# Kernel optimization log

Hardware: AMD Instinct MI355X
Metric: run time of the kernel (lower is better)

## Reference

```python
import jax, jax.numpy as jnp
import numpy as np

B, H, W = 16, 56, 56
CE, CB = 128, 256
NH, WS = 8, 7
HD = CB // NH
N = WS * WS
HID = 4 * CB
EPS = 1e-5


def _rel_pos_index(ws):
    coords = np.stack(np.meshgrid(np.arange(ws), np.arange(ws), indexing='ij')).reshape(2, -1)
    rel = (coords[:, :, None] - coords[:, None, :]).transpose(1, 2, 0).astype(np.int64)
    rel[..., 0] += ws - 1
    rel[..., 1] += ws - 1
    rel[..., 0] *= 2 * ws - 1
    return rel.sum(-1)  # (ws*ws, ws*ws)

RPI = jnp.asarray(_rel_pos_index(WS))


def _ln(x, w, b, axes):
    m = x.mean(axes, keepdims=True)
    v = x.var(axes, keepdims=True)
    return (x - m) * jax.lax.rsqrt(v + EPS) * w + b


def _window_partition(x):  # (B,H,W,C) -> (B*nW, N, C)
    Bx, Hx, Wx, C = x.shape
    x = x.reshape(Bx, Hx // WS, WS, Wx // WS, WS, C)
    return x.transpose(0, 1, 3, 2, 4, 5).reshape(-1, N, C)


def _window_reverse(xw, C):  # (B*nW, N, C) -> (B,H,W,C)
    x = xw.reshape(B, H // WS, W // WS, WS, WS, C)
    return x.transpose(0, 1, 3, 2, 4, 5).reshape(B, H, W, C)


def setup_inputs() -> dict:
    key = jax.random.key(0)
    ks = jax.random.split(key, 12)
    s = 0.02
    return {
        'x_edge': jax.random.normal(ks[0], (B, CE, H, W), jnp.float32),
        'x_body': jax.random.normal(ks[1], (B, H * W, CB), jnp.float32),
        'norm_edge_w': jnp.ones((CE, H, W), jnp.float32),
        'norm_edge_b': jnp.zeros((CE, H, W), jnp.float32),
        'conv_w': jax.random.normal(ks[2], (CB, CE), jnp.float32) * s,
        'norm1_w': jnp.ones((CB,), jnp.float32),
        'norm1_b': jnp.zeros((CB,), jnp.float32),
        'rpb_table': jax.random.normal(ks[3], ((2 * WS - 1) ** 2, NH), jnp.float32) * s,
        'q_w': jax.random.normal(ks[4], (CB, CB), jnp.float32) * s,
        'kv_w': jax.random.normal(ks[5], (2 * CB, CB), jnp.float32) * s,
        'proj_w': jax.random.normal(ks[6], (CB, CB), jnp.float32) * s,
        'proj_b': jnp.zeros((CB,), jnp.float32),
        'norm2_w': jnp.ones((CB,), jnp.float32),
        'norm2_b': jnp.zeros((CB,), jnp.float32),
        'fc1_w': jax.random.normal(ks[7], (HID, CB), jnp.float32) * s,
        'fc1_b': jnp.zeros((HID,), jnp.float32),
        'fc2_w': jax.random.normal(ks[8], (CB, HID), jnp.float32) * s,
        'fc2_b': jnp.zeros((CB,), jnp.float32),
    }


def reference(x_edge, x_body, norm_edge_w, norm_edge_b, conv_w, norm1_w, norm1_b,
              rpb_table, q_w, kv_w, proj_w, proj_b, norm2_w, norm2_b,
              fc1_w, fc1_b, fc2_w, fc2_b):
    x_body_cache = x_body
    scale = HD ** -0.5

    # LayerNorm over (C,H,W) of x_edge, then 1x1 conv (channel mixing), to NHWC
    xe = _ln(x_edge, norm_edge_w, norm_edge_b, axes=(1, 2, 3))  # (B,CE,H,W)
    xe = jnp.einsum('oc,bchw->bhwo', conv_w, xe)                # (B,H,W,CB)

    xb = _ln(x_body, norm1_w, norm1_b, axes=(-1,)).reshape(B, H, W, CB)

    xe_w = _window_partition(xe)  # (Bn,N,CB)
    xb_w = _window_partition(xb)

    q = (xe_w @ q_w.T).reshape(-1, N, NH, HD).transpose(0, 2, 1, 3) * scale  # (Bn,NH,N,HD)
    kv = (xb_w @ kv_w.T).reshape(-1, N, 2, NH, HD).transpose(2, 0, 3, 1, 4)
    k, v = kv[0], kv[1]  # (Bn,NH,N,HD)

    attn = jnp.einsum('bhnd,bhmd->bhnm', q, k)
    bias = rpb_table[RPI.reshape(-1)].reshape(N, N, NH).transpose(2, 0, 1)  # (NH,N,N)
    attn = jax.nn.softmax(attn + bias[None], axis=-1)

    out = jnp.einsum('bhnm,bhmd->bhnd', attn, v).transpose(0, 2, 1, 3).reshape(-1, N, CB)
    out = out @ proj_w.T + proj_b

    x_attn = _window_reverse(out, CB).reshape(B, H * W, CB)
    x = x_body_cache + x_attn

    h = _ln(x, norm2_w, norm2_b, axes=(-1,))
    h = jax.nn.gelu(h @ fc1_w.T + fc1_b, approximate=False) @ fc2_w.T + fc2_b
    x = x + h

    return x.reshape(B, H, W, CB).transpose(0, 3, 1, 2)  # (B,CB,H,W)
```

## Files before the change

kernel.cpp:

```cpp
#include <hip/hip_runtime.h>
#include <hip/hip_bf16.h>
#include <math.h>

#define B_    16
#define CE_   128
#define CB_   256
#define H_    56
#define W_    56
#define NH_   8
#define WS_   7
#define HD_   32
#define NWIN_ 49
#define HW_   3136
#define M_    50176
#define HID_  1024

typedef short bf16x8 __attribute__((ext_vector_type(8)));
typedef float f32x4  __attribute__((ext_vector_type(4)));

__device__ __forceinline__ float waveRedSum(float v) {
#pragma unroll
  for (int off = 32; off; off >>= 1) v += __shfl_xor(v, off, 64);
  return v;
}

__device__ __forceinline__ void load_lds16(const void* g, void* l) {
  __builtin_amdgcn_global_load_lds((__attribute__((address_space(1))) void*)g,
                                   (__attribute__((address_space(3))) void*)l,
                                   16, 0, 0);
}

__global__ void k_stats1(const float* __restrict__ xe, float* __restrict__ part) {
  int blk = blockIdx.x;
  int b = blk >> 6, s = blk & 63;
  const float4* p = (const float4*)(xe + (size_t)b * 401408 + s * 6272);
  float sm = 0.f, s2 = 0.f;
  for (int i = threadIdx.x; i < 1568; i += 256) {
    float4 v = p[i];
    sm += v.x + v.y + v.z + v.w;
    s2 += v.x * v.x + v.y * v.y + v.z * v.z + v.w * v.w;
  }
  sm = waveRedSum(sm); s2 = waveRedSum(s2);
  __shared__ float aux[8];
  int wave = threadIdx.x >> 6, lane = threadIdx.x & 63;
  if (lane == 0) { aux[wave] = sm; aux[4 + wave] = s2; }
  __syncthreads();
  if (threadIdx.x == 0) {
    part[blk * 2]     = aux[0] + aux[1] + aux[2] + aux[3];
    part[blk * 2 + 1] = aux[4] + aux[5] + aux[6] + aux[7];
  }
}

__global__ void k_stats2(const float* __restrict__ part, float* __restrict__ stats) {
  int b = blockIdx.x, lane = threadIdx.x;
  float sm = part[(b * 64 + lane) * 2];
  float s2 = part[(b * 64 + lane) * 2 + 1];
  sm = waveRedSum(sm); s2 = waveRedSum(s2);
  if (lane == 0) {
    float mean = sm / 401408.0f;
    float var  = s2 / 401408.0f - mean * mean;
    stats[b * 2] = mean;
    stats[b * 2 + 1] = rsqrtf(var + 1e-5f);
  }
}

__global__ void k_cast6(const float* __restrict__ s0, const float* __restrict__ s1,
                        const float* __restrict__ s2, const float* __restrict__ s3,
                        const float* __restrict__ s4, const float* __restrict__ s5,
                        __hip_bfloat16* __restrict__ d) {
  size_t i4 = ((size_t)blockIdx.x * 256 + threadIdx.x) * 4;
  if (i4 >= 819200) return;
  const float* src; size_t off;
  if      (i4 < 32768)  { src = s0; off = 0; }
  else if (i4 < 98304)  { src = s1; off = 32768; }
  else if (i4 < 229376) { src = s2; off = 98304; }
  else if (i4 < 294912) { src = s3; off = 229376; }
  else if (i4 < 557056) { src = s4; off = 294912; }
  else                  { src = s5; off = 557056; }
  float4 v = *(const float4*)(src + (i4 - off));
  union { __hip_bfloat16 h[4]; uint2 u; } pk;
  pk.h[0] = __float2bfloat16(v.x);
  pk.h[1] = __float2bfloat16(v.y);
  pk.h[2] = __float2bfloat16(v.z);
  pk.h[3] = __float2bfloat16(v.w);
  *(uint2*)(d + i4) = pk.u;
}

__global__ void k_wqc(const float* __restrict__ qw, const float* __restrict__ cw,
                      __hip_bfloat16* __restrict__ wqc) {
  int o2 = blockIdx.x, c = threadIdx.x;
  float acc = 0.f;
#pragma unroll 4
  for (int o = 0; o < 256; ++o)
    acc += qw[o2 * 256 + o] * cw[o * 128 + c];
  wqc[o2 * 128 + c] = __float2bfloat16(acc * 0.17677669529663687f);
}

__global__ void k_bias_pre(const float* __restrict__ rpb, float* __restrict__ bp) {
  int blk = blockIdx.x;
  int h = blk >> 4, tile = blk & 15;
  int ti = tile >> 2, tj = tile & 3;
  int lane = threadIdx.x;
  int quad = lane >> 4, lm = lane & 15;
  float4 v;
  float* vp = (float*)&v;
#pragma unroll
  for (int r = 0; r < 4; ++r) {
    int i = ti * 16 + quad * 4 + r;
    int j = tj * 16 + lm;
    float b = -1e30f;
    if (i < 49 && j < 49) {
      int rel = (i / 7 - j / 7 + 6) * 13 + (i % 7 - j % 7 + 6);
      b = rpb[rel * 8 + h];
    }
    vp[r] = b;
  }
  *(float4*)&bp[(size_t)(blk * 64 + lane) * 4] = v;
}

__global__ void k_prep_edge(const float* __restrict__ xe,
                            const float* __restrict__ we,
                            const float* __restrict__ be,
                            const float* __restrict__ stats,
                            __hip_bfloat16* __restrict__ Ae) {
  int wb = blockIdx.x;
  int b = wb >> 6, rem = wb & 63;
  int h0 = (rem >> 3) * 7, w0 = (rem & 7) * 7;
  float mean = stats[b * 2], rstd = stats[b * 2 + 1];
  __shared__ __hip_bfloat16 t[49 * 130];
  for (int idx = threadIdx.x; idx < 128 * 49; idx += 256) {
    int c = idx / 49, p = idx % 49;
    int h = h0 + p / 7, w = w0 + p % 7;
    int off = (c * 56 + h) * 56 + w;
    float v = xe[(size_t)b * 401408 + off];
    t[p * 130 + c] = __float2bfloat16((v - mean) * rstd * we[off] + be[off]);
  }
  __syncthreads();
  __hip_bfloat16* dst = Ae + (size_t)wb * 49 * 128;
  for (int idx = threadIdx.x; idx < 49 * 128; idx += 256) {
    int p = idx >> 7, c = idx & 127;
    dst[idx] = t[p * 130 + c];
  }
}

template <bool PERM>
__global__ void k_ln_rows(const float* __restrict__ x,
                          const float* __restrict__ w,
                          const float* __restrict__ bia,
                          __hip_bfloat16* __restrict__ out) {
  int row = blockIdx.x * 4 + (threadIdx.x >> 6);
  int lane = threadIdx.x & 63;
  float4 xv = *(const float4*)(x + (size_t)row * 256 + lane * 4);
  float s  = xv.x + xv.y + xv.z + xv.w;
  float s2 = xv.x * xv.x + xv.y * xv.y + xv.z * xv.z + xv.w * xv.w;
  s = waveRedSum(s); s2 = waveRedSum(s2);
  float mean = s * (1.0f / 256.0f);
  float var  = s2 * (1.0f / 256.0f) - mean * mean;
  float rstd = rsqrtf(var + 1e-5f);
  int orow = row;
  if (PERM) {
    int b = row / 3136, hw = row % 3136;
    int h = hw / 56, ww = hw % 56;
    orow = (b * 64 + (h / 7) * 8 + (ww / 7)) * 49 + (h % 7) * 7 + (ww % 7);
  }
  float4 wv = *(const float4*)(w + lane * 4);
  float4 bv = *(const float4*)(bia + lane * 4);
  union { __hip_bfloat16 h[4]; uint2 u; } pk;
  pk.h[0] = __float2bfloat16((xv.x - mean) * rstd * wv.x + bv.x);
  pk.h[1] = __float2bfloat16((xv.y - mean) * rstd * wv.y + bv.y);
  pk.h[2] = __float2bfloat16((xv.z - mean) * rstd * wv.z + bv.z);
  pk.h[3] = __float2bfloat16((xv.w - mean) * rstd * wv.w + bv.w);
  *(uint2*)(out + (size_t)orow * 256 + lane * 4) = pk.u;
}

template <int EPI, int NX>
__launch_bounds__(256)
__global__ void gemm_bt(const __hip_bfloat16* __restrict__ A,
                        const __hip_bfloat16* __restrict__ Bw,
                        int M, int N, int K,
                        __hip_bfloat16* __restrict__ outb,
                        float* __restrict__ outf,
                        const float* __restrict__ bias,
                        const float* __restrict__ resid) {
  __shared__ __align__(16) char smem[32768];
  __hip_bfloat16* As0 = (__hip_bfloat16*)smem;
  __hip_bfloat16* Bs0 = (__hip_bfloat16*)(smem + 16384);
  const int tid  = threadIdx.x;
  const int lane = tid & 63;
  const int wave = tid >> 6;
  const int quad = lane >> 4;
  const int lm   = lane & 15;
  const int wm   = (wave & 1) << 6;
  const int wn   = (wave >> 1) << 6;
  const int lin  = blockIdx.x;
  const int slot = lin >> 3;
  const int band = (lin & 7) * 49 + slot / NX;
  const int n0   = (slot % NX) * 128;
  const int m0   = band * 128;

  const int rh = (wave & 1) * 64;
  const int qw = wave >> 1;
  const __hip_bfloat16* Arow = A  + (size_t)(m0 + rh + lane) * K;
  const __hip_bfloat16* Brow = Bw + (size_t)(n0 + rh + lane) * K;

  f32x4 acc[4][4];
#pragma unroll
  for (int i = 0; i < 4; ++i)
#pragma unroll
    for (int j = 0; j < 4; ++j)
#pragma unroll
      for (int r = 0; r < 4; ++r) acc[i][j][r] = 0.f;

  auto STAGE = [&](int buf, int k0) {
#pragma unroll
    for (int p = 0; p < 2; ++p) {
      int q = qw + 2 * p;
      load_lds16(Arow + k0 + q * 8, As0 + buf * 4096 + (q * 128 + rh) * 8);
      load_lds16(Brow + k0 + q * 8, Bs0 + buf * 4096 + (q * 128 + rh) * 8);
    }
  };

  const int nt = K >> 5;
  STAGE(0, 0);
  asm volatile("s_waitcnt vmcnt(0)" ::: "memory");
  __builtin_amdgcn_s_barrier();
  __builtin_amdgcn_sched_barrier(0);

  int cur = 0;
  for (int t = 0; t < nt; ++t) {
    if (t + 1 < nt) STAGE(cur ^ 1, (t + 1) << 5);
    bf16x8 af[4], bfr[4];
#pragma unroll
    for (int i = 0; i < 4; ++i)
      af[i] = *(const bf16x8*)(As0 + cur * 4096 + (quad * 128 + wm + i * 16 + lm) * 8);
#pragma unroll
    for (int j = 0; j < 4; ++j)
      bfr[j] = *(const bf16x8*)(Bs0 + cur * 4096 + (quad * 128 + wn + j * 16 + lm) * 8);
#pragma unroll
    for (int i = 0; i < 4; ++i)
#pragma unroll
      for (int j = 0; j < 4; ++j)
        acc[i][j] = __builtin_amdgcn_mfma_f32_16x16x32_bf16(af[i], bfr[j], acc[i][j], 0, 0, 0);
    if (t + 1 < nt) {
      asm volatile("s_waitcnt vmcnt(0)" ::: "memory");
      __builtin_amdgcn_s_barrier();
      __builtin_amdgcn_sched_barrier(0);
    }
    cur ^= 1;
  }

  float* R = (float*)smem;
  const int g    = tid >> 5;
  const int lx   = tid & 31;
  const int half = wave & 1;
  const int gncol = n0 + lx * 4;
  float4 b4;
  if constexpr (EPI != 0) b4 = *(const float4*)&bias[gncol];

#pragma unroll
  for (int i = 0; i < 4; ++i) {
    __syncthreads();
#pragma unroll
    for (int r = 0; r < 4; ++r) {
      const int rl = half * 16 + quad * 4 + r;
#pragma unroll
      for (int j = 0; j < 4; ++j)
        R[rl * 132 + wn + j * 16 + lm] = acc[i][j][r];
    }
    __syncthreads();
#pragma unroll
    for (int p = 0; p < 4; ++p) {
      const int rl = p * 8 + g;
      f32x4 v4 = *(const f32x4*)&R[rl * 132 + lx * 4];
      const int gm = m0 + (rl >> 4) * 64 + i * 16 + (rl & 15);
      if constexpr (EPI == 0) {
        union { __hip_bfloat16 h[4]; uint2 u; } pk;
#pragma unroll
        for (int q2 = 0; q2 < 4; ++q2) pk.h[q2] = __float2bfloat16(v4[q2]);
        *(uint2*)&outb[(size_t)gm * N + gncol] = pk.u;
      } else if constexpr (EPI == 3) {
        union { __hip_bfloat16 h[4]; uint2 u; } pk;
        const float* bp4 = (const float*)&b4;
#pragma unroll
        for (int q2 = 0; q2 < 4; ++q2) {
          float x = v4[q2] + bp4[q2];
          float t = x * fmaf(x * x, -0.10294324f, -2.30220837f);
          float e = __builtin_amdgcn_exp2f(t);
          pk.h[q2] = __float2bfloat16(x * __builtin_amdgcn_rcpf(1.0f + e));
        }
        *(uint2*)&outb[(size_t)gm * N + gncol] = pk.u;
      } else {
        size_t rowbase;
        if constexpr (EPI == 2) {
          int wb = gm / 49, nn = gm % 49;
          int b = wb >> 6, rem = wb & 63;
          int h = (rem >> 3) * 7 + nn / 7, w = (rem & 7) * 7 + nn % 7;
          rowbase = (size_t)(b * 3136 + h * 56 + w) * 256;
        } else {
          rowbase = (size_t)gm * N;
        }
        float4 r4 = *(const float4*)&resid[rowbase + gncol];
        float4 o4;
        o4.x = v4[0] + b4.x + r4.x;
        o4.y = v4[1] + b4.y + r4.y;
        o4.z = v4[2] + b4.z + r4.z;
        o4.w = v4[3] + b4.w + r4.w;
        *(float4*)&outf[rowbase + gncol] = o4;
      }
    }
  }
}

__launch_bounds__(64)
__global__ void k_attn_mfma(const __hip_bfloat16* __restrict__ qb,
                            const __hip_bfloat16* __restrict__ kvb,
                            const float* __restrict__ bp,
                            __hip_bfloat16* __restrict__ ob) {
  int wb = blockIdx.x >> 3;
  int h  = blockIdx.x & 7;
  __shared__ __align__(16) __hip_bfloat16 lds[7424];
  __hip_bfloat16* Qs = lds;
  __hip_bfloat16* Ks = lds + 2560;
  __hip_bfloat16* Vt = lds + 5120;
  __hip_bfloat16* Ps = lds;
  const int lane = threadIdx.x;
  const int quad = lane >> 4, lm = lane & 15;

  const __hip_bfloat16 zb = __float2bfloat16(0.f);
  for (int i = lane; i < 600; i += 64) { Qs[1960 + i] = zb; Ks[1960 + i] = zb; }
  {
    uint4 z; z.x = z.y = z.z = z.w = 0u;
    for (int i = lane; i < 288; i += 64) ((uint4*)Vt)[i] = z;
  }
  {
    int t = lane >> 2, p = lane & 3;
#pragma unroll
    for (int pass = 0; pass < 4; ++pass, t += 16) {
      if (t < 49) {
        size_t rq = (size_t)(wb * 49 + t);
        uint4 qv = *(const uint4*)(qb + rq * 256 + h * 32 + p * 8);
        *(uint4*)&Qs[t * 40 + p * 8] = qv;
        uint4 kv = *(const uint4*)(kvb + rq * 512 + h * 32 + p * 8);
        *(uint4*)&Ks[t * 40 + p * 8] = kv;
        union { uint4 u; __hip_bfloat16 e[8]; } vv;
        vv.u = *(const uint4*)(kvb + rq * 512 + 256 + h * 32 + p * 8);
#pragma unroll
        for (int i = 0; i < 8; ++i) Vt[(p * 8 + i) * 72 + t] = vv.e[i];
      }
    }
  }
  __builtin_amdgcn_s_waitcnt(0);

  bf16x8 qf[4], kf[4];
#pragma unroll
  for (int i = 0; i < 4; ++i) qf[i] = *(const bf16x8*)&Qs[(i * 16 + lm) * 40 + quad * 8];
#pragma unroll
  for (int j = 0; j < 4; ++j) kf[j] = *(const bf16x8*)&Ks[(j * 16 + lm) * 40 + quad * 8];
  f32x4 s[4][4];
#pragma unroll
  for (int i = 0; i < 4; ++i)
#pragma unroll
    for (int j = 0; j < 4; ++j) {
      f32x4 z4; z4[0] = z4[1] = z4[2] = z4[3] = 0.f;
      s[i][j] = __builtin_amdgcn_mfma_f32_16x16x32_bf16(qf[i], kf[j], z4, 0, 0, 0);
    }
#pragma unroll
  for (int ti = 0; ti < 4; ++ti)
#pragma unroll
    for (int tj = 0; tj < 4; ++tj) {
      f32x4 b = *(const f32x4*)&bp[(size_t)(((h * 4 + ti) * 4 + tj) * 64 + lane) * 4];
      s[ti][tj] += b;
    }
  float mrow[4][4], srow[4][4];
#pragma unroll
  for (int ti = 0; ti < 4; ++ti)
#pragma unroll
    for (int r = 0; r < 4; ++r)
      mrow[ti][r] = fmaxf(fmaxf(s[ti][0][r], s[ti][1][r]), fmaxf(s[ti][2][r], s[ti][3][r]));
#pragma unroll
  for (int mask = 1; mask <= 8; mask <<= 1)
#pragma unroll
    for (int ti = 0; ti < 4; ++ti)
#pragma unroll
      for (int r = 0; r < 4; ++r)
        mrow[ti][r] = fmaxf(mrow[ti][r], __shfl_xor(mrow[ti][r], mask, 64));
#pragma unroll
  for (int ti = 0; ti < 4; ++ti)
#pragma unroll
    for (int tj = 0; tj < 4; ++tj)
#pragma unroll
      for (int r = 0; r < 4; ++r)
        s[ti][tj][r] = __expf(s[ti][tj][r] - mrow[ti][r]);
#pragma unroll
  for (int ti = 0; ti < 4; ++ti)
#pragma unroll
    for (int r = 0; r < 4; ++r)
      srow[ti][r] = s[ti][0][r] + s[ti][1][r] + s[ti][2][r] + s[ti][3][r];
#pragma unroll
  for (int mask = 1; mask <= 8; mask <<= 1)
#pragma unroll
    for (int ti = 0; ti < 4; ++ti)
#pragma unroll
      for (int r = 0; r < 4; ++r)
        srow[ti][r] += __shfl_xor(srow[ti][r], mask, 64);
  float inv[4][4];
#pragma unroll
  for (int ti = 0; ti < 4; ++ti)
#pragma unroll
    for (int r = 0; r < 4; ++r)
      inv[ti][r] = 1.0f / srow[ti][r];

#pragma unroll
  for (int ti = 0; ti < 4; ++ti)
#pragma unroll
    for (int tj = 0; tj < 4; ++tj)
#pragma unroll
      for (int r = 0; r < 4; ++r)
        Ps[(ti * 16 + quad * 4 + r) * 72 + tj * 16 + lm] = __float2bfloat16(s[ti][tj][r]);
  __builtin_amdgcn_s_waitcnt(0);

  f32x4 o[4][2];
#pragma unroll
  for (int mt = 0; mt < 4; ++mt)
#pragma unroll
    for (int nt = 0; nt < 2; ++nt)
#pragma unroll
      for (int r = 0; r < 4; ++r) o[mt][nt][r] = 0.f;
#pragma unroll
  for (int kq = 0; kq < 2; ++kq) {
    bf16x8 pa[4], vb[2];
#pragma unroll
    for (int mt = 0; mt < 4; ++mt)
      pa[mt] = *(const bf16x8*)&Ps[(mt * 16 + lm) * 72 + kq * 32 + quad * 8];
#pragma unroll
    for (int nt = 0; nt < 2; ++nt)
      vb[nt] = *(const bf16x8*)&Vt[(nt * 16 + lm) * 72 + kq * 32 + quad * 8];
#pragma unroll
    for (int mt = 0; mt < 4; ++mt)
#pragma unroll
      for (int nt = 0; nt < 2; ++nt)
        o[mt][nt] = __builtin_amdgcn_mfma_f32_16x16x32_bf16(pa[mt], vb[nt], o[mt][nt], 0, 0, 0);
  }
#pragma unroll
  for (int mt = 0; mt < 4; ++mt)
#pragma unroll
    for (int r = 0; r < 4; ++r) {
      int row = mt * 16 + quad * 4 + r;
      if (row < 49) {
#pragma unroll
        for (int nt = 0; nt < 2; ++nt)
          ob[(size_t)(wb * 49 + row) * 256 + h * 32 + nt * 16 + lm] =
              __float2bfloat16(o[mt][nt][r] * inv[mt][r]);
      }
    }
}

__global__ void k_transpose(const float* __restrict__ y, float* __restrict__ out) {
  __shared__ float t[32][33];
  int bb = blockIdx.z;
  int hw0 = blockIdx.x * 32;
  int o0 = blockIdx.y * 32;
  int tx = threadIdx.x, ty = threadIdx.y;
#pragma unroll
  for (int r = 0; r < 4; ++r)
    t[ty + r * 8][tx] = y[(size_t)(bb * 3136 + hw0 + ty + r * 8) * 256 + o0 + tx];
  __syncthreads();
#pragma unroll
  for (int r = 0; r < 4; ++r)
    out[(size_t)(bb * 256 + o0 + ty + r * 8) * 3136 + hw0 + tx] = t[tx][ty + r * 8];
}

extern "C" void kernel_launch(void* const* d_in, const int* in_sizes, int n_in,
                              void* d_out, int out_size, void* d_ws, size_t ws_size,
                              hipStream_t stream) {
  const float* x_edge = (const float*)d_in[0];
  const float* x_body = (const float*)d_in[1];
  const float* ne_w   = (const float*)d_in[2];
  const float* ne_b   = (const float*)d_in[3];
  const float* conv_w = (const float*)d_in[4];
  const float* n1_w   = (const float*)d_in[5];
  const float* n1_b   = (const float*)d_in[6];
  const float* rpb    = (const float*)d_in[7];
  const float* q_w    = (const float*)d_in[8];
  const float* kv_w   = (const float*)d_in[9];
  const float* proj_w = (const float*)d_in[10];
  const float* proj_b = (const float*)d_in[11];
  const float* n2_w   = (const float*)d_in[12];
  const float* n2_b   = (const float*)d_in[13];
  const float* fc1_w  = (const float*)d_in[14];
  const float* fc1_b  = (const float*)d_in[15];
  const float* fc2_w  = (const float*)d_in[16];
  const float* fc2_b  = (const float*)d_in[17];
  float* out = (float*)d_out;
  (void)in_sizes; (void)n_in; (void)out_size; (void)ws_size;

  const size_t SZ_Ae    = (size_t)M_ * 128 * 2;
  const size_t SZ_bf256 = (size_t)M_ * 256 * 2;
  const size_t SZ_bf512 = (size_t)M_ * 512 * 2;
  const size_t SZ_h1    = (size_t)M_ * 1024 * 2;

  char* ws = (char*)d_ws;
  __hip_bfloat16* Wb  = (__hip_bfloat16*)ws;
  float* part  = (float*)(ws + 1638400);
  float* stats = (float*)(ws + 1638400 + 8192);
  float* biasp = (float*)(ws + 1638400 + 8192 + 256);
  __hip_bfloat16* wqc = (__hip_bfloat16*)(ws + 1638400 + 8192 + 256 + 131072);
  char*  P     = ws + 1638400 + 8192 + 256 + 131072 + 65536;
  __hip_bfloat16* w_kv   = Wb + 98304;
  __hip_bfloat16* w_proj = Wb + 229376;
  __hip_bfloat16* w_fc1  = Wb + 294912;
  __hip_bfloat16* w_fc2  = Wb + 557056;
  __hip_bfloat16* Ae    = (__hip_bfloat16*)(P);
  __hip_bfloat16* xbn   = (__hip_bfloat16*)(P + SZ_Ae);
  __hip_bfloat16* qb    = (__hip_bfloat16*)(P + SZ_Ae + SZ_bf256);
  __hip_bfloat16* kvb   = (__hip_bfloat16*)(P + SZ_Ae + 2 * SZ_bf256);
  __hip_bfloat16* attnb = (__hip_bfloat16*)(P + SZ_Ae + 2 * SZ_bf256 + SZ_bf512);
  __hip_bfloat16* h1 = (__hip_bfloat16*)(P);
  char* tail         = P + ((SZ_h1 + 1024 * 1024) & ~(size_t)1023);
  __hip_bfloat16* xn = (__hip_bfloat16*)tail;
  float*          yb = (float*)tail;
  float*          xf = (float*)d_out;

  k_cast6<<<800, 256, 0, stream>>>(conv_w, q_w, kv_w, proj_w, fc1_w, fc2_w, Wb);
  k_wqc<<<256, 128, 0, stream>>>(q_w, conv_w, wqc);
  k_bias_pre<<<128, 64, 0, stream>>>(rpb, biasp);
  k_stats1<<<1024, 256, 0, stream>>>(x_edge, part);
  k_stats2<<<16, 64, 0, stream>>>(part, stats);
  k_prep_edge<<<1024, 256, 0, stream>>>(x_edge, ne_w, ne_b, stats, Ae);
  k_ln_rows<true><<<M_ / 4, 256, 0, stream>>>(x_body, n1_w, n1_b, xbn);
  gemm_bt<0, 2><<<784, 256, 0, stream>>>(Ae, wqc, M_, 256, 128, qb, nullptr, nullptr, nullptr);
  gemm_bt<0, 4><<<1568, 256, 0, stream>>>(xbn, w_kv, M_, 512, 256, kvb, nullptr, nullptr, nullptr);
  k_attn_mfma<<<8192, 64, 0, stream>>>(qb, kvb, biasp, attnb);
  gemm_bt<2, 2><<<784, 256, 0, stream>>>(attnb, w_proj, M_, 256, 256, nullptr, xf, proj_b, x_body);
  k_ln_rows<false><<<M_ / 4, 256, 0, stream>>>(xf, n2_w, n2_b, xn);
  gemm_bt<3, 8><<<3136, 256, 0, stream>>>(xn, w_fc1, M_, 1024, 256, h1, nullptr, fc1_b, nullptr);
  gemm_bt<4, 2><<<784, 256, 0, stream>>>(h1, w_fc2, M_, 256, 1024, nullptr, yb, fc2_b, xf);
  k_transpose<<<dim3(98, 8, 16), dim3(32, 8), 0, stream>>>(yb, out);
}
```

Before: 512.8 us.

## Replace LDS-staged GEMM with direct global-to-register MFMA fragments and 64x256 tiles

The bf16 GEMM kernel no longer stages A and B through double-buffered LDS via global_load_lds. Each wave now loads its MFMA fragments straight from global memory into registers, with two-deep register prefetching. The block tile changes from 128x128 to 64x256, with every wave owning a 64x64 slice of the N dimension. This drops the LDS staging and per-k-step barriers, but the A rows are now read redundantly by all four waves and the global loads are strided and less coalesced, which relies on the L1/L2 caches.

```diff
diff --git a/kernel.cpp b/kernel.cpp
--- a/kernel.cpp
+++ b/kernel.cpp
@@ -22,12 +22,6 @@
 #pragma unroll
   for (int off = 32; off; off >>= 1) v += __shfl_xor(v, off, 64);
   return v;
-}
-
-__device__ __forceinline__ void load_lds16(const void* g, void* l) {
-  __builtin_amdgcn_global_load_lds((__attribute__((address_space(1))) void*)g,
-                                   (__attribute__((address_space(3))) void*)l,
-                                   16, 0, 0);
 }
 
 __global__ void k_stats1(const float* __restrict__ xe, float* __restrict__ part) {
@@ -173,7 +167,7 @@
   *(uint2*)(out + (size_t)orow * 256 + lane * 4) = pk.u;
 }
 
-template <int EPI, int NX>
+template <int EPI, int NXB>
 __launch_bounds__(256)
 __global__ void gemm_bt(const __hip_bfloat16* __restrict__ A,
                         const __hip_bfloat16* __restrict__ Bw,
@@ -182,26 +176,21 @@
                         float* __restrict__ outf,
                         const float* __restrict__ bias,
                         const float* __restrict__ resid) {
-  __shared__ __align__(16) char smem[32768];
-  __hip_bfloat16* As0 = (__hip_bfloat16*)smem;
-  __hip_bfloat16* Bs0 = (__hip_bfloat16*)(smem + 16384);
+  __shared__ __align__(16) float Rw[4 * 16 * 68];
   const int tid  = threadIdx.x;
   const int lane = tid & 63;
   const int wave = tid >> 6;
   const int quad = lane >> 4;
   const int lm   = lane & 15;
-  const int wm   = (wave & 1) << 6;
-  const int wn   = (wave >> 1) << 6;
   const int lin  = blockIdx.x;
   const int slot = lin >> 3;
-  const int band = (lin & 7) * 49 + slot / NX;
-  const int n0   = (slot % NX) * 128;
-  const int m0   = band * 128;
-
-  const int rh = (wave & 1) * 64;
-  const int qw = wave >> 1;
-  const __hip_bfloat16* Arow = A  + (size_t)(m0 + rh + lane) * K;
-  const __hip_bfloat16* Brow = Bw + (size_t)(n0 + rh + lane) * K;
+  const int band = (lin & 7) * 98 + slot / NXB;
+  const int n0w  = (slot % NXB) * 256 + wave * 64;
+  const int m0   = band * 64;
+
+  const __hip_bfloat16* Ab = A  + (size_t)(m0 + lm) * K + quad * 8;
+  const __hip_bfloat16* Bb = Bw + (size_t)(n0w + lm) * K + quad * 8;
+  const size_t sA = (size_t)16 * K;
 
   f32x4 acc[4][4];
 #pragma unroll
@@ -211,73 +200,54 @@
 #pragma unroll
       for (int r = 0; r < 4; ++r) acc[i][j][r] = 0.f;
 
-  auto STAGE = [&](int buf, int k0) {
-#pragma unroll
-    for (int p = 0; p < 2; ++p) {
-      int q = qw + 2 * p;
-      load_lds16(Arow + k0 + q * 8, As0 + buf * 4096 + (q * 128 + rh) * 8);
-      load_lds16(Brow + k0 + q * 8, Bs0 + buf * 4096 + (q * 128 + rh) * 8);
-    }
+  auto LD = [&](bf16x8 (&af)[4], bf16x8 (&bf)[4], int k0) {
+#pragma unroll
+    for (int i = 0; i < 4; ++i) af[i] = *(const bf16x8*)(Ab + k0 + i * sA);
+#pragma unroll
+    for (int j = 0; j < 4; ++j) bf[j] = *(const bf16x8*)(Bb + k0 + j * sA);
   };
+  auto MF = [&](bf16x8 (&af)[4], bf16x8 (&bf)[4]) {
+#pragma unroll
+    for (int i = 0; i < 4; ++i)
+#pragma unroll
+      for (int j = 0; j < 4; ++j)
+        acc[i][j] = __builtin_amdgcn_mfma_f32_16x16x32_bf16(af[i], bf[j], acc[i][j], 0, 0, 0);
+  };
 
   const int nt = K >> 5;
-  STAGE(0, 0);
-  asm volatile("s_waitcnt vmcnt(0)" ::: "memory");
-  __builtin_amdgcn_s_barrier();
-  __builtin_amdgcn_sched_barrier(0);
-
-  int cur = 0;
-  for (int t = 0; t < nt; ++t) {
-    if (t + 1 < nt) STAGE(cur ^ 1, (t + 1) << 5);
-    bf16x8 af[4], bfr[4];
-#pragma unroll
-    for (int i = 0; i < 4; ++i)
-      af[i] = *(const bf16x8*)(As0 + cur * 4096 + (quad * 128 + wm + i * 16 + lm) * 8);
-#pragma unroll
-    for (int j = 0; j < 4; ++j)
-      bfr[j] = *(const bf16x8*)(Bs0 + cur * 4096 + (quad * 128 + wn + j * 16 + lm) * 8);
-#pragma unroll
-    for (int i = 0; i < 4; ++i)
-#pragma unroll
-      for (int j = 0; j < 4; ++j)
-        acc[i][j] = __builtin_amdgcn_mfma_f32_16x16x32_bf16(af[i], bfr[j], acc[i][j], 0, 0, 0);
-    if (t + 1 < nt) {
-      asm volatile("s_waitcnt vmcnt(0)" ::: "memory");
-      __builtin_amdgcn_s_barrier();
-      __builtin_amdgcn_sched_barrier(0);
-    }
-    cur ^= 1;
-  }
-
-  float* R = (float*)smem;
-  const int g    = tid >> 5;
-  const int lx   = tid & 31;
-  const int half = wave & 1;
-  const int gncol = n0 + lx * 4;
+  bf16x8 aX[4], bX[4], aY[4], bY[4];
+  LD(aX, bX, 0);
+  for (int t = 0; t < nt; t += 2) {
+    LD(aY, bY, (t + 1) << 5);
+    MF(aX, bX);
+    if (t + 2 < nt) LD(aX, bX, (t + 2) << 5);
+    MF(aY, bY);
+  }
+
+  float* R = Rw + wave * (16 * 68);
+  const int colg = n0w + lm * 4;
   float4 b4;
-  if constexpr (EPI != 0) b4 = *(const float4*)&bias[gncol];
+  if constexpr (EPI != 0) b4 = *(const float4*)&bias[colg];
 
 #pragma unroll
   for (int i = 0; i < 4; ++i) {
     __syncthreads();
 #pragma unroll
-    for (int r = 0; r < 4; ++r) {
-      const int rl = half * 16 + quad * 4 + r;
+    for (int r = 0; r < 4; ++r)
 #pragma unroll
       for (int j = 0; j < 4; ++j)
-        R[rl * 132 + wn + j * 16 + lm] = acc[i][j][r];
-    }
+        R[(quad * 4 + r) * 68 + j * 16 + lm] = acc[i][j][r];
     __syncthreads();
 #pragma unroll
     for (int p = 0; p < 4; ++p) {
-      const int rl = p * 8 + g;
-      f32x4 v4 = *(const f32x4*)&R[rl * 132 + lx * 4];
-      const int gm = m0 + (rl >> 4) * 64 + i * 16 + (rl & 15);
+      const int row16 = p * 4 + quad;
+      f32x4 v4 = *(const f32x4*)&R[row16 * 68 + lm * 4];
+      const int gm = m0 + i * 16 + row16;
       if constexpr (EPI == 0) {
         union { __hip_bfloat16 h[4]; uint2 u; } pk;
 #pragma unroll
         for (int q2 = 0; q2 < 4; ++q2) pk.h[q2] = __float2bfloat16(v4[q2]);
-        *(uint2*)&outb[(size_t)gm * N + gncol] = pk.u;
+        *(uint2*)&outb[(size_t)gm * N + colg] = pk.u;
       } else if constexpr (EPI == 3) {
         union { __hip_bfloat16 h[4]; uint2 u; } pk;
         const float* bp4 = (const float*)&b4;
@@ -288,7 +258,7 @@
           float e = __builtin_amdgcn_exp2f(t);
           pk.h[q2] = __float2bfloat16(x * __builtin_amdgcn_rcpf(1.0f + e));
         }
-        *(uint2*)&outb[(size_t)gm * N + gncol] = pk.u;
+        *(uint2*)&outb[(size_t)gm * N + colg] = pk.u;
       } else {
         size_t rowbase;
         if constexpr (EPI == 2) {
@@ -299,13 +269,13 @@
         } else {
           rowbase = (size_t)gm * N;
         }
-        float4 r4 = *(const float4*)&resid[rowbase + gncol];
+        float4 r4 = *(const float4*)&resid[rowbase + colg];
         float4 o4;
         o4.x = v4[0] + b4.x + r4.x;
         o4.y = v4[1] + b4.y + r4.y;
         o4.z = v4[2] + b4.z + r4.z;
         o4.w = v4[3] + b4.w + r4.w;
-        *(float4*)&outf[rowbase + gncol] = o4;
+        *(float4*)&outf[rowbase + colg] = o4;
       }
     }
   }
@@ -528,12 +498,12 @@
   k_stats2<<<16, 64, 0, stream>>>(part, stats);
   k_prep_edge<<<1024, 256, 0, stream>>>(x_edge, ne_w, ne_b, stats, Ae);
   k_ln_rows<true><<<M_ / 4, 256, 0, stream>>>(x_body, n1_w, n1_b, xbn);
-  gemm_bt<0, 2><<<784, 256, 0, stream>>>(Ae, wqc, M_, 256, 128, qb, nullptr, nullptr, nullptr);
-  gemm_bt<0, 4><<<1568, 256, 0, stream>>>(xbn, w_kv, M_, 512, 256, kvb, nullptr, nullptr, nullptr);
+  gemm_bt<0, 1><<<784, 256, 0, stream>>>(Ae, wqc, M_, 256, 128, qb, nullptr, nullptr, nullptr);
+  gemm_bt<0, 2><<<1568, 256, 0, stream>>>(xbn, w_kv, M_, 512, 256, kvb, nullptr, nullptr, nullptr);
   k_attn_mfma<<<8192, 64, 0, stream>>>(qb, kvb, biasp, attnb);
-  gemm_bt<2, 2><<<784, 256, 0, stream>>>(attnb, w_proj, M_, 256, 256, nullptr, xf, proj_b, x_body);
+  gemm_bt<2, 1><<<784, 256, 0, stream>>>(attnb, w_proj, M_, 256, 256, nullptr, xf, proj_b, x_body);
   k_ln_rows<false><<<M_ / 4, 256, 0, stream>>>(xf, n2_w, n2_b, xn);
-  gemm_bt<3, 8><<<3136, 256, 0, stream>>>(xn, w_fc1, M_, 1024, 256, h1, nullptr, fc1_b, nullptr);
-  gemm_bt<4, 2><<<784, 256, 0, stream>>>(h1, w_fc2, M_, 256, 1024, nullptr, yb, fc2_b, xf);
+  gemm_bt<3, 4><<<3136, 256, 0, stream>>>(xn, w_fc1, M_, 1024, 256, h1, nullptr, fc1_b, nullptr);
+  gemm_bt<4, 1><<<784, 256, 0, stream>>>(h1, w_fc2, M_, 256, 1024, nullptr, yb, fc2_b, xf);
   k_transpose<<<dim3(98, 8, 16), dim3(32, 8), 0, stream>>>(yb, out);
 }
```

Result: slower. 647.8 us (+26.3%).

## Enlarge GEMM tiles to 256x256 with 512-thread blocks

Applied to the files above, without the earlier changes.

The shared GEMM kernel moves from 128x128 tiles on 256 threads to 256x256 tiles on 512 threads. Each wave now computes a 128x64 sub-tile, the LDS staging buffers double to 64KB, and the epilogue is rewritten to drain 32 rows at a time. The XCD-aware band swizzle of block indices is dropped for a plain linear mapping. Bigger tiles raise arithmetic intensity and cut global reloads, but they also cut the block count: the N=256 GEMMs launch only 196 blocks on a 256-CU device. Register pressure rises too, with 128 accumulator floats per lane.

```diff
diff --git a/kernel.cpp b/kernel.cpp
--- a/kernel.cpp
+++ b/kernel.cpp
@@ -174,7 +174,7 @@
 }
 
 template <int EPI, int NX>
-__launch_bounds__(256)
+__launch_bounds__(512)
 __global__ void gemm_bt(const __hip_bfloat16* __restrict__ A,
                         const __hip_bfloat16* __restrict__ Bw,
                         int M, int N, int K,
@@ -182,41 +182,38 @@
                         float* __restrict__ outf,
                         const float* __restrict__ bias,
                         const float* __restrict__ resid) {
-  __shared__ __align__(16) char smem[32768];
-  __hip_bfloat16* As0 = (__hip_bfloat16*)smem;
-  __hip_bfloat16* Bs0 = (__hip_bfloat16*)(smem + 16384);
+  __shared__ __align__(16) char smem[65536];
   const int tid  = threadIdx.x;
   const int lane = tid & 63;
   const int wave = tid >> 6;
   const int quad = lane >> 4;
   const int lm   = lane & 15;
-  const int wm   = (wave & 1) << 6;
-  const int wn   = (wave >> 1) << 6;
-  const int lin  = blockIdx.x;
-  const int slot = lin >> 3;
-  const int band = (lin & 7) * 49 + slot / NX;
-  const int n0   = (slot % NX) * 128;
-  const int m0   = band * 128;
-
-  const int rh = (wave & 1) * 64;
-  const int qw = wave >> 1;
-  const __hip_bfloat16* Arow = A  + (size_t)(m0 + rh + lane) * K;
-  const __hip_bfloat16* Brow = Bw + (size_t)(n0 + rh + lane) * K;
-
-  f32x4 acc[4][4];
-#pragma unroll
-  for (int i = 0; i < 4; ++i)
+  const int wm2  = (wave & 1) * 128;
+  const int wn2  = (wave >> 1) * 64;
+  const int band = blockIdx.x / NX;
+  const int n0   = (blockIdx.x % NX) * 256;
+  const int m0   = band * 256;
+
+  f32x4 acc[8][4];
+#pragma unroll
+  for (int i = 0; i < 8; ++i)
 #pragma unroll
     for (int j = 0; j < 4; ++j)
 #pragma unroll
       for (int r = 0; r < 4; ++r) acc[i][j][r] = 0.f;
 
+  const int ia0 = wave * 2;
   auto STAGE = [&](int buf, int k0) {
+    __hip_bfloat16* Asb = (__hip_bfloat16*)smem + buf * 16384;
+    __hip_bfloat16* Bsb = Asb + 8192;
 #pragma unroll
     for (int p = 0; p < 2; ++p) {
-      int q = qw + 2 * p;
-      load_lds16(Arow + k0 + q * 8, As0 + buf * 4096 + (q * 128 + rh) * 8);
-      load_lds16(Brow + k0 + q * 8, Bs0 + buf * 4096 + (q * 128 + rh) * 8);
+      int idx = ia0 + p;
+      int qa = idx & 3, rb = idx >> 2;
+      load_lds16(A  + (size_t)(m0 + rb * 64 + lane) * K + k0 + qa * 8,
+                 Asb + (qa * 256 + rb * 64) * 8);
+      load_lds16(Bw + (size_t)(n0 + rb * 64 + lane) * K + k0 + qa * 8,
+                 Bsb + (qa * 256 + rb * 64) * 8);
     }
   };
 
@@ -229,15 +226,17 @@
   int cur = 0;
   for (int t = 0; t < nt; ++t) {
     if (t + 1 < nt) STAGE(cur ^ 1, (t + 1) << 5);
-    bf16x8 af[4], bfr[4];
-#pragma unroll
-    for (int i = 0; i < 4; ++i)
-      af[i] = *(const bf16x8*)(As0 + cur * 4096 + (quad * 128 + wm + i * 16 + lm) * 8);
+    const __hip_bfloat16* Asb = (const __hip_bfloat16*)smem + cur * 16384;
+    const __hip_bfloat16* Bsb = Asb + 8192;
+    bf16x8 af[8], bfr[4];
+#pragma unroll
+    for (int i = 0; i < 8; ++i)
+      af[i] = *(const bf16x8*)&Asb[(quad * 256 + wm2 + i * 16 + lm) * 8];
 #pragma unroll
     for (int j = 0; j < 4; ++j)
-      bfr[j] = *(const bf16x8*)(Bs0 + cur * 4096 + (quad * 128 + wn + j * 16 + lm) * 8);
-#pragma unroll
-    for (int i = 0; i < 4; ++i)
+      bfr[j] = *(const bf16x8*)&Bsb[(quad * 256 + wn2 + j * 16 + lm) * 8];
+#pragma unroll
+    for (int i = 0; i < 8; ++i)
 #pragma unroll
       for (int j = 0; j < 4; ++j)
         acc[i][j] = __builtin_amdgcn_mfma_f32_16x16x32_bf16(af[i], bfr[j], acc[i][j], 0, 0, 0);
@@ -250,29 +249,34 @@
   }
 
   float* R = (float*)smem;
-  const int g    = tid >> 5;
-  const int lx   = tid & 31;
-  const int half = wave & 1;
+  const int lx   = tid & 63;
+  const int g    = tid >> 6;
   const int gncol = n0 + lx * 4;
   float4 b4;
   if constexpr (EPI != 0) b4 = *(const float4*)&bias[gncol];
 
 #pragma unroll
-  for (int i = 0; i < 4; ++i) {
+  for (int pr = 0; pr < 8; ++pr) {
     __syncthreads();
-#pragma unroll
-    for (int r = 0; r < 4; ++r) {
-      const int rl = half * 16 + quad * 4 + r;
-#pragma unroll
-      for (int j = 0; j < 4; ++j)
-        R[rl * 132 + wn + j * 16 + lm] = acc[i][j][r];
+    if ((wave & 1) == (pr >> 2)) {
+#pragma unroll
+      for (int ii = 0; ii < 2; ++ii) {
+        const int i = (pr & 3) * 2 + ii;
+#pragma unroll
+        for (int r = 0; r < 4; ++r) {
+          const int rr = ii * 16 + quad * 4 + r;
+#pragma unroll
+          for (int j = 0; j < 4; ++j)
+            R[rr * 260 + wn2 + j * 16 + lm] = acc[i][j][r];
+        }
+      }
     }
     __syncthreads();
 #pragma unroll
     for (int p = 0; p < 4; ++p) {
-      const int rl = p * 8 + g;
-      f32x4 v4 = *(const f32x4*)&R[rl * 132 + lx * 4];
-      const int gm = m0 + (rl >> 4) * 64 + i * 16 + (rl & 15);
+      const int rr = p * 8 + g;
+      f32x4 v4 = *(const f32x4*)&R[rr * 260 + lx * 4];
+      const int gm = m0 + pr * 32 + rr;
       if constexpr (EPI == 0) {
         union { __hip_bfloat16 h[4]; uint2 u; } pk;
 #pragma unroll
@@ -528,12 +532,12 @@
   k_stats2<<<16, 64, 0, stream>>>(part, stats);
   k_prep_edge<<<1024, 256, 0, stream>>>(x_edge, ne_w, ne_b, stats, Ae);
   k_ln_rows<true><<<M_ / 4, 256, 0, stream>>>(x_body, n1_w, n1_b, xbn);
-  gemm_bt<0, 2><<<784, 256, 0, stream>>>(Ae, wqc, M_, 256, 128, qb, nullptr, nullptr, nullptr);
-  gemm_bt<0, 4><<<1568, 256, 0, stream>>>(xbn, w_kv, M_, 512, 256, kvb, nullptr, nullptr, nullptr);
+  gemm_bt<0, 1><<<196, 512, 0, stream>>>(Ae, wqc, M_, 256, 128, qb, nullptr, nullptr, nullptr);
+  gemm_bt<0, 2><<<392, 512, 0, stream>>>(xbn, w_kv, M_, 512, 256, kvb, nullptr, nullptr, nullptr);
   k_attn_mfma<<<8192, 64, 0, stream>>>(qb, kvb, biasp, attnb);
-  gemm_bt<2, 2><<<784, 256, 0, stream>>>(attnb, w_proj, M_, 256, 256, nullptr, xf, proj_b, x_body);
+  gemm_bt<2, 1><<<196, 512, 0, stream>>>(attnb, w_proj, M_, 256, 256, nullptr, xf, proj_b, x_body);
   k_ln_rows<false><<<M_ / 4, 256, 0, stream>>>(xf, n2_w, n2_b, xn);
-  gemm_bt<3, 8><<<3136, 256, 0, stream>>>(xn, w_fc1, M_, 1024, 256, h1, nullptr, fc1_b, nullptr);
-  gemm_bt<4, 2><<<784, 256, 0, stream>>>(h1, w_fc2, M_, 256, 1024, nullptr, yb, fc2_b, xf);
+  gemm_bt<3, 4><<<784, 512, 0, stream>>>(xn, w_fc1, M_, 1024, 256, h1, nullptr, fc1_b, nullptr);
+  gemm_bt<4, 1><<<196, 512, 0, stream>>>(h1, w_fc2, M_, 256, 1024, nullptr, yb, fc2_b, xf);
   k_transpose<<<dim3(98, 8, 16), dim3(32, 8), 0, stream>>>(yb, out);
 }
```

Measured after the change: 527.7 us. 1.03x slower.
